# Optimization experiments

Hardware: AMD Instinct MI355X
Metric: run time of the kernel (lower is better)

The kernel has to match this reference:

```python
import jax, jax.numpy as jnp
import numpy as np

B, S, D = 1, 2048, 4096
NH, NKV, HD = 32, 8, 128          # n_heads, n_kv_heads, head_dim
N_REP = NH // NKV                  # repeat_kv factor (GQA)
ROPE_THETA = 10000.0


def setup_inputs() -> dict:
    key = jax.random.key(0)
    ks = jax.random.split(key, 5)
    x = jax.random.normal(ks[0], (B, S, D), jnp.float32)
    wq = jax.random.normal(ks[1], (D, NH * HD), jnp.float32) * (1.0 / np.sqrt(D))
    wk = jax.random.normal(ks[2], (D, NKV * HD), jnp.float32) * (1.0 / np.sqrt(D))
    wv = jax.random.normal(ks[3], (D, NKV * HD), jnp.float32) * (1.0 / np.sqrt(D))
    wo = jax.random.normal(ks[4], (NH * HD, D), jnp.float32) * (1.0 / np.sqrt(NH * HD))
    # freqs_cis = exp(i * t * theta^{-2j/hd}); store as cos/sin, shape (S, HD//2)
    inv_freq = 1.0 / (ROPE_THETA ** (np.arange(0, HD, 2, dtype=np.float32) / HD))
    angles = np.outer(np.arange(S, dtype=np.float32), inv_freq)
    return {"x": x, "wq": wq, "wk": wk, "wv": wv, "wo": wo,
            "cos": jnp.asarray(np.cos(angles), jnp.float32),
            "sin": jnp.asarray(np.sin(angles), jnp.float32)}


def _rope(t, cos, sin):
    # t: (b, s, h, hd); pairs (t[...,2j], t[...,2j+1]) form complex numbers
    tr, ti = t[..., 0::2], t[..., 1::2]
    c = cos[None, :, None, :]
    s = sin[None, :, None, :]
    out = jnp.stack([tr * c - ti * s, tr * s + ti * c], axis=-1)  # re-interleave
    return out.reshape(t.shape)


def reference(x, wq, wk, wv, wo, cos, sin):
    b, s, _ = x.shape
    q = (x @ wq).reshape(b, s, NH, HD)
    k = (x @ wk).reshape(b, s, NKV, HD)
    v = (x @ wv).reshape(b, s, NKV, HD)
    q = _rope(q, cos, sin)
    k = _rope(k, cos, sin)
    # prefill with start_pos=0: KV cache slice == fresh k, v
    # repeat_kv == torch.repeat_interleave along head dim
    k = jnp.repeat(k, N_REP, axis=2)  # (b, s, NH, HD)
    v = jnp.repeat(v, N_REP, axis=2)
    q = q.transpose(0, 2, 1, 3)  # (b, NH, s, hd)
    k = k.transpose(0, 2, 1, 3)
    v = v.transpose(0, 2, 1, 3)
    scores = jnp.einsum('bhqd,bhkd->bhqk', q, k) / jnp.sqrt(jnp.float32(HD))
    causal = jnp.tril(jnp.ones((s, s), bool))
    scores = jnp.where(causal[None, None], scores, jnp.float32(-1e30))
    probs = jax.nn.softmax(scores, axis=-1)
    out = jnp.einsum('bhqk,bhkd->bhqd', probs, v)
    out = out.transpose(0, 2, 1, 3).reshape(b, s, NH * HD)
    return out @ wo
```

## Files before the change

### kernel.cpp

```cpp
#include <hip/hip_runtime.h>
#include <stdint.h>

typedef unsigned short ushort_t;
typedef short bf16x4 __attribute__((ext_vector_type(4)));
typedef short bf16x8 __attribute__((ext_vector_type(8)));
typedef float f32x4 __attribute__((ext_vector_type(4)));
typedef float f32x16 __attribute__((ext_vector_type(16)));
typedef float f32x4v __attribute__((ext_vector_type(4)));

__device__ __forceinline__ ushort_t f2bf(float f) {
  unsigned int u = __builtin_bit_cast(unsigned int, f);
  u += 0x7fffu + ((u >> 16) & 1u);
  return (ushort_t)(u >> 16);
}
__device__ __forceinline__ float bf2f(ushort_t h) {
  unsigned int u = ((unsigned int)h) << 16;
  return __builtin_bit_cast(float, u);
}
__device__ __forceinline__ float exp2_hw(float x) {
  return __builtin_amdgcn_exp2f(x);
}
__device__ __forceinline__ void load_lds16(const void* g, void* l) {
  __builtin_amdgcn_global_load_lds(
      (const __attribute__((address_space(1))) void*)g,
      (__attribute__((address_space(3))) void*)l, 16, 0, 0);
}

__global__ __launch_bounds__(256) void cvt_x_kernel(const float* __restrict__ x,
                                                    ushort_t* __restrict__ xb) {
  int i = blockIdx.x * 256 + threadIdx.x;
  const f32x4v* xv = (const f32x4v*)x;
  f32x4v a = xv[2 * i], b = xv[2 * i + 1];
  bf16x8 o;
  o[0] = (short)f2bf(a[0]); o[1] = (short)f2bf(a[1]);
  o[2] = (short)f2bf(a[2]); o[3] = (short)f2bf(a[3]);
  o[4] = (short)f2bf(b[0]); o[5] = (short)f2bf(b[1]);
  o[6] = (short)f2bf(b[2]); o[7] = (short)f2bf(b[3]);
  ((bf16x8*)xb)[i] = o;
}

__global__ __launch_bounds__(256) void tr_cvt_kernel(const float* __restrict__ src,
                                                     ushort_t* __restrict__ dst,
                                                     int R, int C) {
  __shared__ float tile[64][65];
  int r0 = blockIdx.y * 64, c0 = blockIdx.x * 64;
  int t = threadIdx.x;
#pragma unroll
  for (int i = 0; i < 4; i++) {
    int idx = t + i * 256;
    int r = idx >> 4, c4 = idx & 15;
    f32x4v v = *(const f32x4v*)&src[(size_t)(r0 + r) * C + c0 + c4 * 4];
#pragma unroll
    for (int j = 0; j < 4; j++) tile[r][c4 * 4 + j] = v[j];
  }
  __syncthreads();
#pragma unroll
  for (int i = 0; i < 4; i++) {
    int idx = t + i * 256;
    int cr = idx >> 4, cg = idx & 15;
    bf16x4 o;
#pragma unroll
    for (int j = 0; j < 4; j++) o[j] = (short)f2bf(tile[cg * 4 + j][cr]);
    *(bf16x4*)&dst[(size_t)(c0 + cr) * R + r0 + cg * 4] = o;
  }
}

__global__ __launch_bounds__(256) void rope_kernel(ushort_t* __restrict__ C1,
                                                   const float* __restrict__ cosb,
                                                   const float* __restrict__ sinb) {
  int idx = blockIdx.x * 256 + threadIdx.x;
  int s = idx / 640;
  int col0 = (idx % 640) * 8;
  int i0 = (col0 & 127) >> 1;
  const float qs = (col0 < 4096) ? 0.12753055296570565f : 1.0f;
  ushort_t* p = C1 + (size_t)s * 6144 + col0;
  bf16x8 v = *(const bf16x8*)p;
  bf16x8 o;
  const float* cr = cosb + s * 64 + i0;
  const float* sr = sinb + s * 64 + i0;
#pragma unroll
  for (int j = 0; j < 4; j++) {
    float tr = bf2f((ushort_t)v[2 * j]);
    float ti = bf2f((ushort_t)v[2 * j + 1]);
    float c = cr[j], sn = sr[j];
    o[2 * j] = (short)f2bf((tr * c - ti * sn) * qs);
    o[2 * j + 1] = (short)f2bf((tr * sn + ti * c) * qs);
  }
  *(bf16x8*)p = o;
}

__global__ __launch_bounds__(256) void trv_kernel(const ushort_t* __restrict__ C1,
                                                  ushort_t* __restrict__ VT) {
  __shared__ ushort_t tile[64][65];
  int c0 = blockIdx.x * 64;
  int r0 = blockIdx.y * 64;
  int t = threadIdx.x;
#pragma unroll
  for (int i = 0; i < 16; i++) {
    int idx = t + i * 256;
    int r = idx >> 6, c = idx & 63;
    tile[r][c] = C1[(size_t)(r0 + r) * 6144 + 5120 + c0 + c];
  }
  __syncthreads();
#pragma unroll
  for (int i = 0; i < 16; i++) {
    int idx = t + i * 256;
    int cr = idx >> 6, cc = idx & 63;
    VT[(size_t)(c0 + cr) * 2048 + r0 + cc] = tile[cc][cr];
  }
}

__device__ __forceinline__ void xcd_chunk_map(int id, int nby, int nbx,
                                              int& browi, int& bcoli) {
  const int xcd = id & 7;
  const int j = id >> 3;
  const int rch = nby >> 1, cch = nbx >> 2;
  const int cr = xcd >> 2, cc = xcd & 3;
  const int r = j / cch, c = j % cch;
  browi = cr * rch + r;
  bcoli = cc * cch + c;
}

template <typename OutT>
__global__ __launch_bounds__(512) void gemmC_kernel(const ushort_t* __restrict__ A,
                                                    const ushort_t* __restrict__ BT,
                                                    OutT* __restrict__ C,
                                                    int M, int N, int K, int ldc) {
  __shared__ ushort_t As[2][256 * 64];
  __shared__ ushort_t Bs[3][192 * 64];
  const int nbx = N / 192, nby = M >> 8;
  int browi, bcoli;
  xcd_chunk_map((int)blockIdx.x, nby, nbx, browi, bcoli);
  const int brow = browi << 8, bcol = bcoli * 192;
  const int tid = threadIdx.x, w = tid >> 6, lane = tid & 63;
  const int wr = w >> 2, wc = w & 3;
  const int lr = lane & 15, lk = lane >> 4;

  const ushort_t* Ab = A + (size_t)brow * K;
  const ushort_t* Bb = BT + (size_t)bcol * K;

  auto stageQ = [&](const ushort_t* gbase, char* lds, int t, int q) {
    int L = q * 512 + tid;
    int r = L >> 3, sc = L & 7;
    load_lds16(gbase + (size_t)r * K + (t << 6) + ((sc ^ (r & 7)) << 3), lds + L * 16);
  };

  f32x4 acc[8][3] = {};
  const int NT = K >> 6;

#pragma unroll
  for (int q = 0; q < 3; ++q) stageQ(Bb, (char*)&Bs[0][0], 0, q);
  stageQ(Ab, (char*)&As[0][0], 0, 0);
  stageQ(Ab, (char*)&As[0][0], 0, 2);
  stageQ(Ab, (char*)&As[0][0], 0, 1);
  stageQ(Ab, (char*)&As[0][0], 0, 3);
#pragma unroll
  for (int q = 0; q < 3; ++q) stageQ(Bb, (char*)&Bs[1][0], 1, q);
  asm volatile("s_waitcnt vmcnt(5)" ::: "memory");
  __builtin_amdgcn_s_barrier();

  int bcur = 0;
  for (int t = 0; t < NT; ++t) {
    const int c = t & 1;
    const char* Ac = (const char*)&As[c][0];
    const char* Bc = (const char*)&Bs[bcur][0];
    char* An = (char*)&As[c ^ 1][0];
    const int bnxt = (bcur + 2 >= 3) ? bcur - 1 : bcur + 2;
    char* Bn = (char*)&Bs[bnxt][0];
    const bool pfA = (t + 1 < NT), pfB = (t + 2 < NT);

    bf16x8 af[4][2], bfr[3][2];
#pragma unroll
    for (int mm = 0; mm < 4; ++mm)
#pragma unroll
      for (int ks = 0; ks < 2; ++ks) {
        int rA = wr * 128 + mm * 16 + lr;
        af[mm][ks] = *(const bf16x8*)(Ac + rA * 128 + (((ks * 4 + lk) ^ (rA & 7)) << 4));
      }
#pragma unroll
    for (int n = 0; n < 2; ++n)
#pragma unroll
      for (int ks = 0; ks < 2; ++ks) {
        int rB = wc * 48 + n * 16 + lr;
        bfr[n][ks] = *(const bf16x8*)(Bc + rB * 128 + (((ks * 4 + lk) ^ (rB & 7)) << 4));
      }
    if (pfA) { stageQ(Ab, An, t + 1, 0); stageQ(Ab, An, t + 1, 2); }
    __builtin_amdgcn_s_barrier();
    asm volatile("s_waitcnt lgkmcnt(0)" ::: "memory");
    __builtin_amdgcn_sched_barrier(0);
    __builtin_amdgcn_s_setprio(1);
#pragma unroll
    for (int mm = 0; mm < 4; ++mm)
#pragma unroll
      for (int n = 0; n < 2; ++n)
#pragma unroll
        for (int ks = 0; ks < 2; ++ks)
          acc[mm][n] = __builtin_amdgcn_mfma_f32_16x16x32_bf16(af[mm][ks], bfr[n][ks],
                                                               acc[mm][n], 0, 0, 0);
    __builtin_amdgcn_s_setprio(0);
    __builtin_amdgcn_s_barrier();

#pragma unroll
    for (int ks = 0; ks < 2; ++ks) {
      int rB = wc * 48 + 32 + lr;
      bfr[2][ks] = *(const bf16x8*)(Bc + rB * 128 + (((ks * 4 + lk) ^ (rB & 7)) << 4));
    }
    if (pfA) { stageQ(Ab, An, t + 1, 1); stageQ(Ab, An, t + 1, 3); }
    __builtin_amdgcn_s_barrier();
    asm volatile("s_waitcnt lgkmcnt(0)" ::: "memory");
    __builtin_amdgcn_sched_barrier(0);
    __builtin_amdgcn_s_setprio(1);
#pragma unroll
    for (int mm = 0; mm < 4; ++mm)
#pragma unroll
      for (int ks = 0; ks < 2; ++ks)
        acc[mm][2] = __builtin_amdgcn_mfma_f32_16x16x32_bf16(af[mm][ks], bfr[2][ks],
                                                             acc[mm][2], 0, 0, 0);
    __builtin_amdgcn_s_setprio(0);
    asm volatile("s_waitcnt vmcnt(7)" ::: "memory");
    __builtin_amdgcn_s_barrier();

#pragma unroll
    for (int mm = 0; mm < 4; ++mm)
#pragma unroll
      for (int ks = 0; ks < 2; ++ks) {
        int rA = wr * 128 + 64 + mm * 16 + lr;
        af[mm][ks] = *(const bf16x8*)(Ac + rA * 128 + (((ks * 4 + lk) ^ (rA & 7)) << 4));
      }
    if (pfB) { stageQ(Bb, Bn, t + 2, 0); stageQ(Bb, Bn, t + 2, 1); }
    __builtin_amdgcn_s_barrier();
    asm volatile("s_waitcnt lgkmcnt(0)" ::: "memory");
    __builtin_amdgcn_sched_barrier(0);
    __builtin_amdgcn_s_setprio(1);
#pragma unroll
    for (int mm = 0; mm < 4; ++mm)
#pragma unroll
      for (int n = 0; n < 2; ++n)
#pragma unroll
        for (int ks = 0; ks < 2; ++ks)
          acc[4 + mm][n] = __builtin_amdgcn_mfma_f32_16x16x32_bf16(af[mm][ks], bfr[n][ks],
                                                                   acc[4 + mm][n], 0, 0, 0);
    __builtin_amdgcn_s_setprio(0);
    __builtin_amdgcn_s_barrier();

    if (pfB) stageQ(Bb, Bn, t + 2, 2);
    __builtin_amdgcn_s_setprio(1);
#pragma unroll
    for (int mm = 0; mm < 4; ++mm)
#pragma unroll
      for (int ks = 0; ks < 2; ++ks)
        acc[4 + mm][2] = __builtin_amdgcn_mfma_f32_16x16x32_bf16(af[mm][ks], bfr[2][ks],
                                                                 acc[4 + mm][2], 0, 0, 0);
    __builtin_amdgcn_s_setprio(0);
    if (pfB)
      asm volatile("s_waitcnt vmcnt(5)" ::: "memory");
    else
      asm volatile("s_waitcnt vmcnt(0)" ::: "memory");
    __builtin_amdgcn_s_barrier();
    bcur = (bcur + 1 == 3) ? 0 : bcur + 1;
  }
#pragma unroll
  for (int m = 0; m < 8; ++m)
#pragma unroll
    for (int n = 0; n < 3; ++n) {
      int row = brow + wr * 128 + m * 16 + lk * 4;
      int col = bcol + wc * 48 + n * 16 + lr;
#pragma unroll
      for (int j = 0; j < 4; ++j) {
        float v = acc[m][n][j];
        if constexpr (sizeof(OutT) == 2)
          C[(size_t)(row + j) * ldc + col] = (OutT)f2bf(v);
        else
          C[(size_t)(row + j) * ldc + col] = v;
      }
    }
}

template <typename OutT>
__global__ __launch_bounds__(512) void gemmB_kernel(const ushort_t* __restrict__ A,
                                                    const ushort_t* __restrict__ BT,
                                                    OutT* __restrict__ C,
                                                    int M, int N, int K, int ldc) {
  __shared__ ushort_t As[3][128 * 64];
  __shared__ ushort_t Bs[3][256 * 64];
  const int nbx = N >> 8, nby = M >> 7;
  int browi, bcoli;
  xcd_chunk_map((int)blockIdx.x, nby, nbx, browi, bcoli);
  const int brow = browi << 7, bcol = bcoli << 8;
  const int tid = threadIdx.x, w = tid >> 6, lane = tid & 63;
  const int wr = w >> 2, wc = w & 3;
  const int lr = lane & 15, lk = lane >> 4;

  const ushort_t* Ab = A + (size_t)brow * K;
  const ushort_t* Bb = BT + (size_t)bcol * K;

  auto stageQ = [&](const ushort_t* gbase, char* lds, int t, int q) {
    int L = q * 512 + tid;
    int r = L >> 3, sc = L & 7;
    load_lds16(gbase + (size_t)r * K + (t << 6) + ((sc ^ (r & 7)) << 3), lds + L * 16);
  };
  auto stageTile = [&](int t, int buf) {
    stageQ(Ab, (char*)&As[buf][0], t, 0);
    stageQ(Ab, (char*)&As[buf][0], t, 1);
#pragma unroll
    for (int q = 0; q < 4; ++q) stageQ(Bb, (char*)&Bs[buf][0], t, q);
  };

  f32x4 acc[4][4] = {};
  const int NT = K >> 6;

  stageTile(0, 0);
  stageTile(1, 1);
  asm volatile("s_waitcnt vmcnt(6)" ::: "memory");
  __builtin_amdgcn_s_barrier();

  int cur = 0;
  for (int t = 0; t < NT; ++t) {
    const char* Ac = (const char*)&As[cur][0];
    const char* Bc = (const char*)&Bs[cur][0];
    const int nxt = (cur + 2 >= 3) ? cur - 1 : cur + 2;
    char* An = (char*)&As[nxt][0];
    char* Bn = (char*)&Bs[nxt][0];
    const bool pf = (t + 2 < NT);

    bf16x8 af[4][2], bfr[4][2];
#pragma unroll
    for (int mm = 0; mm < 2; ++mm)
#pragma unroll
      for (int ks = 0; ks < 2; ++ks) {
        int rA = wr * 64 + mm * 16 + lr;
        af[mm][ks] = *(const bf16x8*)(Ac + rA * 128 + (((ks * 4 + lk) ^ (rA & 7)) << 4));
      }
#pragma unroll
    for (int n = 0; n < 2; ++n)
#pragma unroll
      for (int ks = 0; ks < 2; ++ks) {
        int rB = wc * 64 + n * 16 + lr;
        bfr[n][ks] = *(const bf16x8*)(Bc + rB * 128 + (((ks * 4 + lk) ^ (rB & 7)) << 4));
      }
    if (pf) stageQ(Ab, An, t + 2, 0);
    __builtin_amdgcn_s_barrier();
    asm volatile("s_waitcnt lgkmcnt(0)" ::: "memory");
    __builtin_amdgcn_sched_barrier(0);
    __builtin_amdgcn_s_setprio(1);
#pragma unroll
    for (int mm = 0; mm < 2; ++mm)
#pragma unroll
      for (int n = 0; n < 2; ++n)
#pragma unroll
        for (int ks = 0; ks < 2; ++ks)
          acc[mm][n] = __builtin_amdgcn_mfma_f32_16x16x32_bf16(af[mm][ks], bfr[n][ks],
                                                               acc[mm][n], 0, 0, 0);
    __builtin_amdgcn_s_setprio(0);
    __builtin_amdgcn_s_barrier();

#pragma unroll
    for (int n = 2; n < 4; ++n)
#pragma unroll
      for (int ks = 0; ks < 2; ++ks) {
        int rB = wc * 64 + n * 16 + lr;
        bfr[n][ks] = *(const bf16x8*)(Bc + rB * 128 + (((ks * 4 + lk) ^ (rB & 7)) << 4));
      }
    if (pf) stageQ(Ab, An, t + 2, 1);
    __builtin_amdgcn_s_barrier();
    asm volatile("s_waitcnt lgkmcnt(0)" ::: "memory");
    __builtin_amdgcn_sched_barrier(0);
    __builtin_amdgcn_s_setprio(1);
#pragma unroll
    for (int mm = 0; mm < 2; ++mm)
#pragma unroll
      for (int n = 2; n < 4; ++n)
#pragma unroll
        for (int ks = 0; ks < 2; ++ks)
          acc[mm][n] = __builtin_amdgcn_mfma_f32_16x16x32_bf16(af[mm][ks], bfr[n][ks],
                                                               acc[mm][n], 0, 0, 0);
    __builtin_amdgcn_s_setprio(0);
    __builtin_amdgcn_s_barrier();

#pragma unroll
    for (int mm = 0; mm < 2; ++mm)
#pragma unroll
      for (int ks = 0; ks < 2; ++ks) {
        int rA = wr * 64 + (mm + 2) * 16 + lr;
        af[2 + mm][ks] = *(const bf16x8*)(Ac + rA * 128 + (((ks * 4 + lk) ^ (rA & 7)) << 4));
      }
    if (pf) { stageQ(Bb, Bn, t + 2, 0); stageQ(Bb, Bn, t + 2, 1); }
    __builtin_amdgcn_s_barrier();
    asm volatile("s_waitcnt lgkmcnt(0)" ::: "memory");
    __builtin_amdgcn_sched_barrier(0);
    __builtin_amdgcn_s_setprio(1);
#pragma unroll
    for (int mm = 0; mm < 2; ++mm)
#pragma unroll
      for (int n = 0; n < 2; ++n)
#pragma unroll
        for (int ks = 0; ks < 2; ++ks)
          acc[2 + mm][n] = __builtin_amdgcn_mfma_f32_16x16x32_bf16(af[2 + mm][ks], bfr[n][ks],
                                                                   acc[2 + mm][n], 0, 0, 0);
    __builtin_amdgcn_s_setprio(0);
    __builtin_amdgcn_s_barrier();

    if (pf) { stageQ(Bb, Bn, t + 2, 2); stageQ(Bb, Bn, t + 2, 3); }
    __builtin_amdgcn_s_setprio(1);
#pragma unroll
    for (int mm = 0; mm < 2; ++mm)
#pragma unroll
      for (int n = 2; n < 4; ++n)
#pragma unroll
        for (int ks = 0; ks < 2; ++ks)
          acc[2 + mm][n] = __builtin_amdgcn_mfma_f32_16x16x32_bf16(af[2 + mm][ks], bfr[n][ks],
                                                                   acc[2 + mm][n], 0, 0, 0);
    __builtin_amdgcn_s_setprio(0);
    if (pf)
      asm volatile("s_waitcnt vmcnt(6)" ::: "memory");
    else if (t + 1 < NT)
      asm volatile("s_waitcnt vmcnt(0)" ::: "memory");
    __builtin_amdgcn_s_barrier();
    cur = (cur == 2) ? 0 : cur + 1;
  }
#pragma unroll
  for (int m = 0; m < 4; ++m)
#pragma unroll
    for (int n = 0; n < 4; ++n) {
      int row = brow + wr * 64 + m * 16 + lk * 4;
      int col = bcol + wc * 64 + n * 16 + lr;
#pragma unroll
      for (int j = 0; j < 4; ++j) {
        float v = acc[m][n][j];
        if constexpr (sizeof(OutT) == 2)
          C[(size_t)(row + j) * ldc + col] = (OutT)f2bf(v);
        else
          C[(size_t)(row + j) * ldc + col] = v;
      }
    }
}

template <typename OutT>
__global__ __launch_bounds__(256) void gemm128_kernel(const ushort_t* __restrict__ A,
                                                      const ushort_t* __restrict__ BT,
                                                      OutT* __restrict__ C,
                                                      int M, int N, int K, int ldc) {
  __shared__ ushort_t As[128 * 32];
  __shared__ ushort_t Bs[128 * 32];
  int brow = blockIdx.y * 128, bcol = blockIdx.x * 128;
  int tid = threadIdx.x, w = tid >> 6, lane = tid & 63;
  int wr = w >> 1, wc = w & 1;
  int lr = lane & 15, lk = lane >> 4;
  f32x4 acc[4][4] = {};

  int srow = lane >> 2;
  int scol = (lane & 3) * 8;
  const ushort_t* Ab = A + (size_t)brow * K + scol;
  const ushort_t* Bb = BT + (size_t)bcol * K + scol;

  for (int kt = 0; kt < K; kt += 32) {
#pragma unroll
    for (int i = 0; i < 2; i++) {
      int seg = w * 2 + i;
      int row = seg * 16 + srow;
      load_lds16(Ab + (size_t)row * K + kt, (char*)As + seg * 1024);
      load_lds16(Bb + (size_t)row * K + kt, (char*)Bs + seg * 1024);
    }
    __syncthreads();
    bf16x8 af[4], bfr[4];
#pragma unroll
    for (int m = 0; m < 4; m++)
      af[m] = *(const bf16x8*)&As[(wr * 64 + m * 16 + lr) * 32 + lk * 8];
#pragma unroll
    for (int n = 0; n < 4; n++)
      bfr[n] = *(const bf16x8*)&Bs[(wc * 64 + n * 16 + lr) * 32 + lk * 8];
#pragma unroll
    for (int m = 0; m < 4; m++)
#pragma unroll
      for (int n = 0; n < 4; n++)
        acc[m][n] = __builtin_amdgcn_mfma_f32_16x16x32_bf16(af[m], bfr[n], acc[m][n], 0, 0, 0);
    __syncthreads();
  }
#pragma unroll
  for (int m = 0; m < 4; m++)
#pragma unroll
    for (int n = 0; n < 4; n++) {
      int row = brow + wr * 64 + m * 16 + lk * 4;
      int col = bcol + wc * 64 + n * 16 + lr;
#pragma unroll
      for (int j = 0; j < 4; j++) {
        float v = acc[m][n][j];
        if constexpr (sizeof(OutT) == 2)
          C[(size_t)(row + j) * ldc + col] = (OutT)f2bf(v);
        else
          C[(size_t)(row + j) * ldc + col] = v;
      }
    }
}

__global__ __launch_bounds__(256) void gemmS_kernel(const ushort_t* __restrict__ C1,
                                                    ushort_t* __restrict__ P) {
  int rem = blockIdx.x, rt = 0;
  while (rem > rt) { rem -= (rt + 1); rt++; }
  const int ct = rem;
  const int h = blockIdx.y, hk = h >> 2;

  __shared__ ushort_t As[128 * 32];
  __shared__ ushort_t Bs[128 * 32];
  int tid = threadIdx.x, w = tid >> 6, lane = tid & 63;
  int wr = w >> 1, wc = w & 1;
  int lr = lane & 15, lk = lane >> 4;
  f32x4 acc[4][4] = {};
  int srow = lane >> 2;
  int scol = (lane & 3) * 8;
  const ushort_t* Ab = C1 + (size_t)(rt * 128) * 6144 + h * 128 + scol;
  const ushort_t* Bb = C1 + (size_t)(ct * 128) * 6144 + 4096 + hk * 128 + scol;

  for (int kt = 0; kt < 128; kt += 32) {
#pragma unroll
    for (int i = 0; i < 2; i++) {
      int seg = w * 2 + i;
      int row = seg * 16 + srow;
      load_lds16(Ab + (size_t)row * 6144 + kt, (char*)As + seg * 1024);
      load_lds16(Bb + (size_t)row * 6144 + kt, (char*)Bs + seg * 1024);
    }
    __syncthreads();
    bf16x8 af[4], bfr[4];
#pragma unroll
    for (int m = 0; m < 4; m++)
      af[m] = *(const bf16x8*)&As[(wr * 64 + m * 16 + lr) * 32 + lk * 8];
#pragma unroll
    for (int n = 0; n < 4; n++)
      bfr[n] = *(const bf16x8*)&Bs[(wc * 64 + n * 16 + lr) * 32 + lk * 8];
#pragma unroll
    for (int m = 0; m < 4; m++)
#pragma unroll
      for (int n = 0; n < 4; n++)
        acc[m][n] = __builtin_amdgcn_mfma_f32_16x16x32_bf16(af[m], bfr[n], acc[m][n], 0, 0, 0);
    __syncthreads();
  }
  ushort_t* Pt = P + ((size_t)h * 136 + (size_t)(rt * (rt + 1) / 2) + ct) * 16384;
  const bool diag = (rt == ct);
#pragma unroll
  for (int m = 0; m < 4; m++)
#pragma unroll
    for (int n = 0; n < 4; n++) {
      int row = wr * 64 + m * 16 + lk * 4;
      int col = wc * 64 + n * 16 + lr;
#pragma unroll
      for (int j = 0; j < 4; j++) {
        float v = exp2_hw(acc[m][n][j]);
        if (diag && col > row + j) v = 0.f;
        Pt[(row + j) * 128 + col] = f2bf(v);
      }
    }
}

__global__ __launch_bounds__(256) void gemmPV_kernel(const ushort_t* __restrict__ P,
                                                     const ushort_t* __restrict__ VT,
                                                     ushort_t* __restrict__ AO) {
  const int h = blockIdx.x, hk = h >> 2;
  const int rt = 15 - (int)blockIdx.y;

  __shared__ ushort_t As[128 * 32];
  __shared__ ushort_t Bs[128 * 32];
  int tid = threadIdx.x, w = tid >> 6, lane = tid & 63;
  int wr = w >> 1, wc = w & 1;
  int lr = lane & 15, lk = lane >> 4;
  f32x4 acc[4][4] = {};
  f32x4 sacc[4] = {};
  bf16x8 ones;
#pragma unroll
  for (int j = 0; j < 8; j++) ones[j] = (short)0x3F80;
  int srow = lane >> 2;
  int scol = (lane & 3) * 8;
  const ushort_t* Ph = P + ((size_t)h * 136 + (size_t)(rt * (rt + 1) / 2)) * 16384;
  const ushort_t* Vh = VT + (size_t)hk * 128 * 2048;

  const int nks = (rt + 1) * 4;
  for (int ks = 0; ks < nks; ks++) {
    int k0 = ks * 32;
    int ctk = k0 >> 7, kin = k0 & 127;
#pragma unroll
    for (int i = 0; i < 2; i++) {
      int seg = w * 2 + i;
      int row = seg * 16 + srow;
      load_lds16(Ph + (size_t)ctk * 16384 + (size_t)row * 128 + kin + scol,
                 (char*)As + seg * 1024);
      load_lds16(Vh + (size_t)row * 2048 + k0 + scol, (char*)Bs + seg * 1024);
    }
    __syncthreads();
    bf16x8 af[4], bfr[4];
#pragma unroll
    for (int m = 0; m < 4; m++)
      af[m] = *(const bf16x8*)&As[(wr * 64 + m * 16 + lr) * 32 + lk * 8];
#pragma unroll
    for (int n = 0; n < 4; n++)
      bfr[n] = *(const bf16x8*)&Bs[(wc * 64 + n * 16 + lr) * 32 + lk * 8];
#pragma unroll
    for (int m = 0; m < 4; m++) {
#pragma unroll
      for (int n = 0; n < 4; n++)
        acc[m][n] = __builtin_amdgcn_mfma_f32_16x16x32_bf16(af[m], bfr[n], acc[m][n], 0, 0, 0);
      sacc[m] = __builtin_amdgcn_mfma_f32_16x16x32_bf16(af[m], ones, sacc[m], 0, 0, 0);
    }
    __syncthreads();
  }
  const int q0 = rt * 128;
#pragma unroll
  for (int m = 0; m < 4; m++) {
    float invs[4];
#pragma unroll
    for (int j = 0; j < 4; j++) invs[j] = 1.0f / sacc[m][j];
#pragma unroll
    for (int n = 0; n < 4; n++) {
      int row = wr * 64 + m * 16 + lk * 4;
      int col = wc * 64 + n * 16 + lr;
#pragma unroll
      for (int j = 0; j < 4; j++) {
        float v = acc[m][n][j] * invs[j];
        AO[(size_t)(q0 + row + j) * 4096 + h * 128 + col] = f2bf(v);
      }
    }
  }
}

__global__ __launch_bounds__(256) void fattn_kernel(const ushort_t* __restrict__ C1,
                                                    const ushort_t* __restrict__ VT,
                                                    ushort_t* __restrict__ AO) {
  __shared__ ushort_t Pl[4][32][72];
  const int h = blockIdx.x, hk = h >> 2;
  const int qt = gridDim.y - 1 - blockIdx.y;
  const int tid = threadIdx.x, w = tid >> 6, lane = tid & 63;
  const int lq = lane & 31, hi = lane >> 5;
  const int qw0 = qt * 128 + w * 32;
  const int qabs = qw0 + lq;

  const ushort_t* Kb = C1 + 4096 + (size_t)hk * 128;
  const ushort_t* Vb = VT + (size_t)hk * 128 * 2048;

  bf16x8 qf[8];
  {
    const ushort_t* qrow = C1 + (size_t)qabs * 6144 + h * 128;
#pragma unroll
    for (int s = 0; s < 8; s++) qf[s] = *(const bf16x8*)(qrow + s * 16 + hi * 8);
  }
  f32x16 ot[4] = {};
  float mrow = -1e30f, ssum = 0.f;

  const int ktmax = (qw0 + 31) >> 6;
  for (int kt = 0; kt <= ktmax; kt++) {
    f32x16 sg[2] = {};
#pragma unroll
    for (int g = 0; g < 2; g++) {
      bf16x8 kfa[8];
      const ushort_t* krow = Kb + (size_t)(kt * 64 + g * 32 + lq) * 6144 + hi * 8;
#pragma unroll
      for (int s = 0; s < 8; s++) kfa[s] = *(const bf16x8*)(krow + s * 16);
#pragma unroll
      for (int s = 0; s < 8; s++)
        sg[g] = __builtin_amdgcn_mfma_f32_32x32x16_bf16(kfa[s], qf[s], sg[g], 0, 0, 0);
    }
    if (kt * 64 + 63 > qw0) {
#pragma unroll
      for (int g = 0; g < 2; g++)
#pragma unroll
        for (int r = 0; r < 16; r++) {
          int key = kt * 64 + g * 32 + (r & 3) + 8 * (r >> 2) + 4 * hi;
          if (key > qabs) sg[g][r] = -1e30f;
        }
    }
    float pm = -1e30f;
#pragma unroll
    for (int g = 0; g < 2; g++)
#pragma unroll
      for (int r = 0; r < 16; r++) pm = fmaxf(pm, sg[g][r]);
    pm = fmaxf(pm, __shfl_xor(pm, 32));
    float mnew = fmaxf(mrow, pm);
    float corr = exp2_hw(mrow - mnew);
    mrow = mnew;
    float ps = 0.f;
#pragma unroll
    for (int g = 0; g < 2; g++)
#pragma unroll
      for (int r = 0; r < 16; r++) {
        float e = exp2_hw(sg[g][r] - mnew);
        sg[g][r] = e;
        ps += e;
      }
    ps += __shfl_xor(ps, 32);
    ssum = ssum * corr + ps;
    if (!__all(corr == 1.f)) {
#pragma unroll
      for (int d = 0; d < 4; d++)
#pragma unroll
        for (int r = 0; r < 16; r++) ot[d][r] *= corr;
    }
#pragma unroll
    for (int g = 0; g < 2; g++)
#pragma unroll
      for (int rq = 0; rq < 4; rq++) {
        bf16x4 pk;
#pragma unroll
        for (int j = 0; j < 4; j++) pk[j] = (short)f2bf(sg[g][rq * 4 + j]);
        *(bf16x4*)&Pl[w][lq][g * 32 + rq * 8 + hi * 4] = pk;
      }
    asm volatile("s_waitcnt lgkmcnt(0)" ::: "memory");
    bf16x8 pf[4];
#pragma unroll
    for (int s = 0; s < 4; s++) pf[s] = *(const bf16x8*)&Pl[w][lq][s * 16 + hi * 8];
#pragma unroll
    for (int d = 0; d < 4; d++) {
      bf16x8 vfa[4];
      const ushort_t* vrow = Vb + (size_t)(d * 32 + lq) * 2048 + kt * 64 + hi * 8;
#pragma unroll
      for (int s = 0; s < 4; s++) vfa[s] = *(const bf16x8*)(vrow + s * 16);
#pragma unroll
      for (int s = 0; s < 4; s++)
        ot[d] = __builtin_amdgcn_mfma_f32_32x32x16_bf16(vfa[s], pf[s], ot[d], 0, 0, 0);
    }
  }
  const float inv = 1.0f / ssum;
  ushort_t* orow = AO + (size_t)qabs * 4096 + h * 128;
#pragma unroll
  for (int d = 0; d < 4; d++)
#pragma unroll
    for (int rq = 0; rq < 4; rq++) {
      bf16x4 ok;
#pragma unroll
      for (int j = 0; j < 4; j++) ok[j] = (short)f2bf(ot[d][rq * 4 + j] * inv);
      *(bf16x4*)(orow + d * 32 + rq * 8 + hi * 4) = ok;
    }
}

extern "C" void kernel_launch(void* const* d_in, const int* in_sizes, int n_in,
                              void* d_out, int out_size, void* d_ws, size_t ws_size,
                              hipStream_t stream) {
  (void)in_sizes; (void)n_in; (void)out_size;
  const float* x    = (const float*)d_in[0];
  const float* wq   = (const float*)d_in[1];
  const float* wk   = (const float*)d_in[2];
  const float* wv   = (const float*)d_in[3];
  const float* wo   = (const float*)d_in[4];
  const float* cosb = (const float*)d_in[5];
  const float* sinb = (const float*)d_in[6];

  char* ws = (char*)d_ws;
  const bool fast = ws_size >= (215ull << 20);

  if (fast) {
    ushort_t* C1  = (ushort_t*)(ws);
    ushort_t* VT  = (ushort_t*)(ws + ((size_t)24 << 20));
    ushort_t* woT = (ushort_t*)(ws + ((size_t)28 << 20));
    ushort_t* xb  = (ushort_t*)(ws + ((size_t)60 << 20));
    ushort_t* wT  = (ushort_t*)(ws + ((size_t)76 << 20));
    ushort_t* P   = (ushort_t*)(ws + ((size_t)60 << 20));
    ushort_t* AO  = (ushort_t*)(ws + ((size_t)196 << 20));

    cvt_x_kernel<<<4096, 256, 0, stream>>>(x, xb);
    tr_cvt_kernel<<<dim3(64, 64), 256, 0, stream>>>(wq, wT, 4096, 4096);
    tr_cvt_kernel<<<dim3(16, 64), 256, 0, stream>>>(wk, wT + (size_t)4096 * 4096, 4096, 1024);
    tr_cvt_kernel<<<dim3(16, 64), 256, 0, stream>>>(wv, wT + (size_t)5120 * 4096, 4096, 1024);
    tr_cvt_kernel<<<dim3(64, 64), 256, 0, stream>>>(wo, woT, 4096, 4096);

    gemmC_kernel<ushort_t><<<256, 512, 0, stream>>>(xb, wT, C1, 2048, 6144, 4096, 6144);
    rope_kernel<<<5120, 256, 0, stream>>>(C1, cosb, sinb);
    trv_kernel<<<dim3(16, 32), 256, 0, stream>>>(C1, VT);

    gemmS_kernel<<<dim3(136, 32), 256, 0, stream>>>(C1, P);
    gemmPV_kernel<<<dim3(32, 16), 256, 0, stream>>>(P, VT, AO);

    gemmB_kernel<float><<<256, 512, 0, stream>>>(AO, woT, (float*)d_out, 2048, 4096, 4096, 4096);
  } else {
    ushort_t* xb  = (ushort_t*)(ws);
    ushort_t* wT  = (ushort_t*)(ws + ((size_t)16 << 20));
    ushort_t* C1  = (ushort_t*)(ws + ((size_t)64 << 20));
    ushort_t* VT  = (ushort_t*)(ws + ((size_t)88 << 20));
    ushort_t* AO  = xb;
    ushort_t* woT = wT;

    cvt_x_kernel<<<4096, 256, 0, stream>>>(x, xb);
    tr_cvt_kernel<<<dim3(64, 64), 256, 0, stream>>>(wq, wT, 4096, 4096);
    tr_cvt_kernel<<<dim3(16, 64), 256, 0, stream>>>(wk, wT + (size_t)4096 * 4096, 4096, 1024);
    tr_cvt_kernel<<<dim3(16, 64), 256, 0, stream>>>(wv, wT + (size_t)5120 * 4096, 4096, 1024);
    gemm128_kernel<ushort_t><<<dim3(48, 16), 256, 0, stream>>>(xb, wT, C1, 2048, 6144, 4096, 6144);
    rope_kernel<<<5120, 256, 0, stream>>>(C1, cosb, sinb);
    trv_kernel<<<dim3(16, 32), 256, 0, stream>>>(C1, VT);
    tr_cvt_kernel<<<dim3(64, 64), 256, 0, stream>>>(wo, woT, 4096, 4096);
    fattn_kernel<<<dim3(32, 16), 256, 0, stream>>>(C1, VT, AO);
    gemm128_kernel<float><<<dim3(32, 16), 256, 0, stream>>>(AO, woT, (float*)d_out, 2048, 4096, 4096, 4096);
  }
}
```

Before: 373.4 us.

## Fuse RoPE and Q scaling into QKV GEMM epilogue; retile output projection GEMM

Applies rotary embedding and the Q softmax pre-scale inside the QKV projection GEMM epilogue. Each element gets its rotation partner from the adjacent lane via a shuffle, which removes the separate rope_kernel pass over Q/K. The output projection GEMM also changes its block tile from 128x256 to 256x128, with a simpler two-phase staging/MFMA schedule. The epilogue now does per-element cos/sin loads, which adds memory traffic at the end of the GEMM.

```diff
diff --git a/kernel.cpp b/kernel.cpp
--- a/kernel.cpp
+++ b/kernel.cpp
@@ -121,11 +121,12 @@
   bcoli = cc * cch + c;
 }
 
-template <typename OutT>
 __global__ __launch_bounds__(512) void gemmC_kernel(const ushort_t* __restrict__ A,
                                                     const ushort_t* __restrict__ BT,
-                                                    OutT* __restrict__ C,
-                                                    int M, int N, int K, int ldc) {
+                                                    ushort_t* __restrict__ C,
+                                                    int M, int N, int K, int ldc,
+                                                    const float* __restrict__ cosb,
+                                                    const float* __restrict__ sinb) {
   __shared__ ushort_t As[2][256 * 64];
   __shared__ ushort_t Bs[3][192 * 64];
   const int nbx = N / 192, nby = M >> 8;
@@ -259,6 +260,7 @@
     __builtin_amdgcn_s_barrier();
     bcur = (bcur + 1 == 3) ? 0 : bcur + 1;
   }
+  const float QS = 0.12753055296570565f;
 #pragma unroll
   for (int m = 0; m < 8; ++m)
 #pragma unroll
@@ -268,25 +270,33 @@
 #pragma unroll
       for (int j = 0; j < 4; ++j) {
         float v = acc[m][n][j];
-        if constexpr (sizeof(OutT) == 2)
-          C[(size_t)(row + j) * ldc + col] = (OutT)f2bf(v);
-        else
-          C[(size_t)(row + j) * ldc + col] = v;
+        float p = __shfl_xor(v, 1, 64);
+        float outv;
+        if (col < 5120) {
+          int i0 = (col & 127) >> 1;
+          int r = row + j;
+          float cv = cosb[r * 64 + i0], sv = sinb[r * 64 + i0];
+          float ro = v * cv + ((col & 1) ? p * sv : -p * sv);
+          outv = (col < 4096) ? ro * QS : ro;
+        } else {
+          outv = v;
+        }
+        C[(size_t)(row + j) * ldc + col] = f2bf(outv);
       }
     }
 }
 
 template <typename OutT>
-__global__ __launch_bounds__(512) void gemmB_kernel(const ushort_t* __restrict__ A,
+__global__ __launch_bounds__(512) void gemmD_kernel(const ushort_t* __restrict__ A,
                                                     const ushort_t* __restrict__ BT,
                                                     OutT* __restrict__ C,
                                                     int M, int N, int K, int ldc) {
-  __shared__ ushort_t As[3][128 * 64];
-  __shared__ ushort_t Bs[3][256 * 64];
-  const int nbx = N >> 8, nby = M >> 7;
+  __shared__ ushort_t As[3][256 * 64];
+  __shared__ ushort_t Bs[3][128 * 64];
+  const int nbx = N >> 7, nby = M >> 8;
   int browi, bcoli;
   xcd_chunk_map((int)blockIdx.x, nby, nbx, browi, bcoli);
-  const int brow = browi << 7, bcol = bcoli << 8;
+  const int brow = browi << 8, bcol = bcoli << 7;
   const int tid = threadIdx.x, w = tid >> 6, lane = tid & 63;
   const int wr = w >> 2, wc = w & 3;
   const int lr = lane & 15, lk = lane >> 4;
@@ -300,13 +310,13 @@
     load_lds16(gbase + (size_t)r * K + (t << 6) + ((sc ^ (r & 7)) << 3), lds + L * 16);
   };
   auto stageTile = [&](int t, int buf) {
-    stageQ(Ab, (char*)&As[buf][0], t, 0);
-    stageQ(Ab, (char*)&As[buf][0], t, 1);
-#pragma unroll
-    for (int q = 0; q < 4; ++q) stageQ(Bb, (char*)&Bs[buf][0], t, q);
+#pragma unroll
+    for (int q = 0; q < 4; ++q) stageQ(Ab, (char*)&As[buf][0], t, q);
+#pragma unroll
+    for (int q = 0; q < 2; ++q) stageQ(Bb, (char*)&Bs[buf][0], t, q);
   };
 
-  f32x4 acc[4][4] = {};
+  f32x4 acc[8][2] = {};
   const int NT = K >> 6;
 
   stageTile(0, 0);
@@ -323,28 +333,28 @@
     char* Bn = (char*)&Bs[nxt][0];
     const bool pf = (t + 2 < NT);
 
-    bf16x8 af[4][2], bfr[4][2];
-#pragma unroll
-    for (int mm = 0; mm < 2; ++mm)
+    bf16x8 af[4][2], bfr[2][2];
+#pragma unroll
+    for (int mm = 0; mm < 4; ++mm)
 #pragma unroll
       for (int ks = 0; ks < 2; ++ks) {
-        int rA = wr * 64 + mm * 16 + lr;
+        int rA = wr * 128 + mm * 16 + lr;
         af[mm][ks] = *(const bf16x8*)(Ac + rA * 128 + (((ks * 4 + lk) ^ (rA & 7)) << 4));
       }
 #pragma unroll
     for (int n = 0; n < 2; ++n)
 #pragma unroll
       for (int ks = 0; ks < 2; ++ks) {
-        int rB = wc * 64 + n * 16 + lr;
+        int rB = wc * 32 + n * 16 + lr;
         bfr[n][ks] = *(const bf16x8*)(Bc + rB * 128 + (((ks * 4 + lk) ^ (rB & 7)) << 4));
       }
-    if (pf) stageQ(Ab, An, t + 2, 0);
+    if (pf) { stageQ(Ab, An, t + 2, 0); stageQ(Ab, An, t + 2, 2); stageQ(Bb, Bn, t + 2, 0); }
     __builtin_amdgcn_s_barrier();
     asm volatile("s_waitcnt lgkmcnt(0)" ::: "memory");
     __builtin_amdgcn_sched_barrier(0);
     __builtin_amdgcn_s_setprio(1);
 #pragma unroll
-    for (int mm = 0; mm < 2; ++mm)
+    for (int mm = 0; mm < 4; ++mm)
 #pragma unroll
       for (int n = 0; n < 2; ++n)
 #pragma unroll
@@ -355,61 +365,25 @@
     __builtin_amdgcn_s_barrier();
 
 #pragma unroll
-    for (int n = 2; n < 4; ++n)
+    for (int mm = 0; mm < 4; ++mm)
 #pragma unroll
       for (int ks = 0; ks < 2; ++ks) {
-        int rB = wc * 64 + n * 16 + lr;
-        bfr[n][ks] = *(const bf16x8*)(Bc + rB * 128 + (((ks * 4 + lk) ^ (rB & 7)) << 4));
-      }
-    if (pf) stageQ(Ab, An, t + 2, 1);
+        int rA = wr * 128 + 64 + mm * 16 + lr;
+        af[mm][ks] = *(const bf16x8*)(Ac + rA * 128 + (((ks * 4 + lk) ^ (rA & 7)) << 4));
+      }
+    if (pf) { stageQ(Ab, An, t + 2, 1); stageQ(Ab, An, t + 2, 3); stageQ(Bb, Bn, t + 2, 1); }
     __builtin_amdgcn_s_barrier();
     asm volatile("s_waitcnt lgkmcnt(0)" ::: "memory");
     __builtin_amdgcn_sched_barrier(0);
     __builtin_amdgcn_s_setprio(1);
 #pragma unroll
-    for (int mm = 0; mm < 2; ++mm)
-#pragma unroll
-      for (int n = 2; n < 4; ++n)
+    for (int mm = 0; mm < 4; ++mm)
+#pragma unroll
+      for (int n = 0; n < 2; ++n)
 #pragma unroll
         for (int ks = 0; ks < 2; ++ks)
-          acc[mm][n] = __builtin_amdgcn_mfma_f32_16x16x32_bf16(af[mm][ks], bfr[n][ks],
-                                                               acc[mm][n], 0, 0, 0);
-    __builtin_amdgcn_s_setprio(0);
-    __builtin_amdgcn_s_barrier();
-
-#pragma unroll
-    for (int mm = 0; mm < 2; ++mm)
-#pragma unroll
-      for (int ks = 0; ks < 2; ++ks) {
-        int rA = wr * 64 + (mm + 2) * 16 + lr;
-        af[2 + mm][ks] = *(const bf16x8*)(Ac + rA * 128 + (((ks * 4 + lk) ^ (rA & 7)) << 4));
-      }
-    if (pf) { stageQ(Bb, Bn, t + 2, 0); stageQ(Bb, Bn, t + 2, 1); }
-    __builtin_amdgcn_s_barrier();
-    asm volatile("s_waitcnt lgkmcnt(0)" ::: "memory");
-    __builtin_amdgcn_sched_barrier(0);
-    __builtin_amdgcn_s_setprio(1);
-#pragma unroll
-    for (int mm = 0; mm < 2; ++mm)
-#pragma unroll
-      for (int n = 0; n < 2; ++n)
-#pragma unroll
-        for (int ks = 0; ks < 2; ++ks)
-          acc[2 + mm][n] = __builtin_amdgcn_mfma_f32_16x16x32_bf16(af[2 + mm][ks], bfr[n][ks],
-                                                                   acc[2 + mm][n], 0, 0, 0);
-    __builtin_amdgcn_s_setprio(0);
-    __builtin_amdgcn_s_barrier();
-
-    if (pf) { stageQ(Bb, Bn, t + 2, 2); stageQ(Bb, Bn, t + 2, 3); }
-    __builtin_amdgcn_s_setprio(1);
-#pragma unroll
-    for (int mm = 0; mm < 2; ++mm)
-#pragma unroll
-      for (int n = 2; n < 4; ++n)
-#pragma unroll
-        for (int ks = 0; ks < 2; ++ks)
-          acc[2 + mm][n] = __builtin_amdgcn_mfma_f32_16x16x32_bf16(af[2 + mm][ks], bfr[n][ks],
-                                                                   acc[2 + mm][n], 0, 0, 0);
+          acc[4 + mm][n] = __builtin_amdgcn_mfma_f32_16x16x32_bf16(af[mm][ks], bfr[n][ks],
+                                                                   acc[4 + mm][n], 0, 0, 0);
     __builtin_amdgcn_s_setprio(0);
     if (pf)
       asm volatile("s_waitcnt vmcnt(6)" ::: "memory");
@@ -419,11 +393,11 @@
     cur = (cur == 2) ? 0 : cur + 1;
   }
 #pragma unroll
-  for (int m = 0; m < 4; ++m)
-#pragma unroll
-    for (int n = 0; n < 4; ++n) {
-      int row = brow + wr * 64 + m * 16 + lk * 4;
-      int col = bcol + wc * 64 + n * 16 + lr;
+  for (int m = 0; m < 8; ++m)
+#pragma unroll
+    for (int n = 0; n < 2; ++n) {
+      int row = brow + wr * 128 + m * 16 + lk * 4;
+      int col = bcol + wc * 32 + n * 16 + lr;
 #pragma unroll
       for (int j = 0; j < 4; ++j) {
         float v = acc[m][n][j];
@@ -758,14 +732,13 @@
     tr_cvt_kernel<<<dim3(16, 64), 256, 0, stream>>>(wv, wT + (size_t)5120 * 4096, 4096, 1024);
     tr_cvt_kernel<<<dim3(64, 64), 256, 0, stream>>>(wo, woT, 4096, 4096);
 
-    gemmC_kernel<ushort_t><<<256, 512, 0, stream>>>(xb, wT, C1, 2048, 6144, 4096, 6144);
-    rope_kernel<<<5120, 256, 0, stream>>>(C1, cosb, sinb);
+    gemmC_kernel<<<256, 512, 0, stream>>>(xb, wT, C1, 2048, 6144, 4096, 6144, cosb, sinb);
     trv_kernel<<<dim3(16, 32), 256, 0, stream>>>(C1, VT);
 
     gemmS_kernel<<<dim3(136, 32), 256, 0, stream>>>(C1, P);
     gemmPV_kernel<<<dim3(32, 16), 256, 0, stream>>>(P, VT, AO);
 
-    gemmB_kernel<float><<<256, 512, 0, stream>>>(AO, woT, (float*)d_out, 2048, 4096, 4096, 4096);
+    gemmD_kernel<float><<<256, 512, 0, stream>>>(AO, woT, (float*)d_out, 2048, 4096, 4096, 4096);
   } else {
     ushort_t* xb  = (ushort_t*)(ws);
     ushort_t* wT  = (ushort_t*)(ws + ((size_t)16 << 20));
```

After: 372.0 us. About the same (-0.4%).
